# Performance work log

Measured on AMD Instinct MI355X. Metric: run time of the kernel, lower is better.

The kernel has to match this reference:

```python
import jax, jax.numpy as jnp
import numpy as np

T, B, P, D = 64, 32, 9, 512  # turns, batch, parties(=N_s), D_u=D_k=D_h


def setup_inputs() -> dict:
    key = jax.random.key(0)
    ks = jax.random.split(key, 12)
    f = lambda k, s: jax.random.normal(k, s, dtype=jnp.float32)
    sc = 0.02
    spk = jax.random.randint(ks[5], (T, B), 0, P)
    return {
        "U": f(ks[0], (T, B, D)), "SK": f(ks[1], (T, B, D)),
        "NU": f(ks[2], (T, B, D)), "LK": f(ks[3], (T, B, D)),
        "A": f(ks[4], (T, B, D)),
        "qmask": jax.nn.one_hot(spk, P, dtype=jnp.float32),  # one-hot party mask [T,B,P]
        # 4 Attention blocks (state11,state12,state21,state22): w_k, w_q, proj (D->D each)
        "Wk": f(ks[6], (4, D, D)) * sc, "bk": jnp.zeros((4, D), jnp.float32),
        "Wq": f(ks[7], (4, D, D)) * sc, "bq": jnp.zeros((4, D), jnp.float32),
        "Wp": f(ks[8], (4, D, D)) * sc, "bp": jnp.zeros((4, D), jnp.float32),
        # per-speaker GRUCell weights (dict of GRUCells -> stacked [P, ...], torch gate order r,z,n)
        "Wih": f(ks[9], (P, 3 * D, D)) * sc, "Whh": f(ks[10], (P, 3 * D, D)) * sc,
        "bih": jnp.zeros((P, 3 * D), jnp.float32), "bhh": jnp.zeros((P, 3 * D), jnp.float32),
    }


def reference(U, SK, NU, LK, A, qmask, Wk, bk, Wq, bq, Wp, bp, Wih, Whh, bih, bhh):
    Tn, Bn, Dn = U.shape
    Pn = qmask.shape[-1]
    bidx = jnp.arange(Bn)

    def attn(i, k2, q2):
        # Attention(D_k), n_head=1, score_function='dot_product', dropout=0 (eval)
        kx = k2 @ Wk[i].T + bk[i]                 # [B, D]
        qx = q2 @ Wq[i].T + bq[i]                 # [B, D]
        # k_len=q_len=1 -> score = <qx_b, kx_b>; original softmaxes over dim=0 (the batch axis!)
        score = jax.nn.softmax(jnp.sum(qx * kx, axis=-1), axis=0)  # [B]
        return (score[:, None] * kx) @ Wp[i].T + bp[i]  # [B, D]

    def gru(x, h, idx):
        # dynamically-routed per-speaker GRUCell: gather speaker weights, batched matvec
        gi = jnp.einsum('bd,bkd->bk', x, Wih[idx]) + bih[idx]  # [B, 3D]
        gh = jnp.einsum('bd,bkd->bk', h, Whh[idx]) + bhh[idx]
        ir, iz, inn = jnp.split(gi, 3, axis=-1)
        hr, hz, hn = jnp.split(gh, 3, axis=-1)
        r = jax.nn.sigmoid(ir + hr)
        z = jax.nn.sigmoid(iz + hz)
        n = jnp.tanh(inn + r * hn)
        return (1.0 - z) * n + z * h

    # qmask_n[t] = qmask[t+1] (next speaker), last repeats
    qmask_n = jnp.concatenate([qmask[1:], qmask[-1:]], axis=0)

    def step(s, xs):
        u, sk, nu, lk, qm, qmn = xs
        qi = jnp.argmax(qm, axis=1)   # speaker id per sample
        qni = jnp.argmax(qmn, axis=1)  # listener (next speaker) id
        s0s = s[bidx, qi]              # _select_parties
        s0l = s[bidx, qni]
        s_0 = attn(0, sk, u)
        s_s = attn(1, sk, s_0)
        s_1 = attn(2, lk, nu)
        s_l = attn(3, lk, s_1)
        spk = gru(s_s, s0s, qi)        # speaker state update
        lst = gru(s_l, s0l, qni)       # listener state update
        s_full = jnp.zeros_like(s).at[bidx, qi].set(spk)   # scatter_ dim=1
        l_full = jnp.zeros_like(s).at[bidx, qni].set(lst)
        s_new = (s * (1.0 - qm[..., None] - qmn[..., None])
                 + s_full * qm[..., None] + l_full * qmn[..., None])
        return s_new, s_new[bidx, qi]  # emit selected speaker state

    s0 = jnp.zeros((Bn, Pn, Dn), U.dtype)
    _, outs = jax.lax.scan(step, s0, (U, SK, NU, LK, qmask, qmask_n))
    # s_ starts as zeros(1, B, D_h) and concatenates per-step selections -> [T+1, B, D]
    return jnp.concatenate([jnp.zeros((1, Bn, Dn), U.dtype), outs], axis=0)
```

## Files before the change

### kernel.cpp

```cpp
#include <hip/hip_runtime.h>
#include <math.h>

#define Tn 64
#define Bn 32
#define Pn 9
#define Dn 512
#define TBn 2048
#define G3 1536
#define NCH 16

using short8 = __attribute__((ext_vector_type(8))) short;
using f32x4  = __attribute__((ext_vector_type(4))) float;
typedef unsigned long long ull;
typedef unsigned int uint;

__device__ __forceinline__ float fsigmoid(float x){ return 1.0f/(1.0f+__expf(-x)); }
__device__ __forceinline__ ushort f2bf(float x){
  unsigned u = __float_as_uint(x);
  return (ushort)((u + 0x7FFFu + ((u>>16)&1u)) >> 16);
}
__device__ __forceinline__ float bf2f(ushort h){
  return __uint_as_float(((unsigned)h)<<16);
}
__device__ __forceinline__ uint pk32(float x){
  ushort h = f2bf(x);
  ushort l = f2bf(x - bf2f(h));
  return ((uint)h << 16) | (uint)l;
}

__device__ __forceinline__ ull ld_agent8(const ull* p){
  return __hip_atomic_load(p, __ATOMIC_RELAXED, __HIP_MEMORY_SCOPE_AGENT);
}
__device__ __forceinline__ void st_agent8(ull* p, ull v){
  __hip_atomic_store(p, v, __ATOMIC_RELAXED, __HIP_MEMORY_SCOPE_AGENT);
}
__device__ __forceinline__ unsigned ld_agent4(const int* p){
  return (unsigned)__hip_atomic_load(p, __ATOMIC_RELAXED, __HIP_MEMORY_SCOPE_AGENT);
}
__device__ __forceinline__ void st_agent4(int* p, int v){
  __hip_atomic_store(p, v, __ATOMIC_RELAXED, __HIP_MEMORY_SCOPE_AGENT);
}
__device__ __forceinline__ float ulo(ull v){ return __uint_as_float((unsigned)v); }
__device__ __forceinline__ float uhi(ull v){ return __uint_as_float((unsigned)(v>>32)); }
__device__ __forceinline__ ull upack(float a, float b){
  return ((ull)__float_as_uint(b) << 32) | (ull)__float_as_uint(a);
}

__global__ void k_prep(const float* __restrict__ qmask, int* __restrict__ qi,
                       int* __restrict__ qni, float* __restrict__ h0A,
                       float* __restrict__ h0B, float* __restrict__ out,
                       int* __restrict__ counts, int* __restrict__ lists,
                       int* __restrict__ dcnt, int* __restrict__ dlist,
                       int* __restrict__ rowflag){
  int t = blockIdx.x; int tid = threadIdx.x;
  int gidx = blockIdx.x*256 + tid;
  if (gidx < 16) counts[gidx] = 0;
  if (gidx < Bn*Pn*NCH) st_agent4(&rowflag[gidx], 0);
  for (int i=gidx; i<9*4096; i+=64*256) lists[i] = -1;
  __shared__ int qis[32], qnis[32];
  __shared__ int cnt9[9];
  if (tid < 9) cnt9[tid] = 0;
  if (tid < Bn){
    int b = tid;
    const float* qm = qmask + ((size_t)t*Bn + b)*Pn;
    int best = 0; float bv = qm[0];
    #pragma unroll
    for (int p=1;p<Pn;p++){ float v=qm[p]; if (v>bv){bv=v;best=p;} }
    qi[t*Bn+b] = best; qis[b] = best;
    int tn = (t==Tn-1)? t : t+1;
    const float* qmn = qmask + ((size_t)tn*Bn + b)*Pn;
    best = 0; bv = qmn[0];
    #pragma unroll
    for (int p=1;p<Pn;p++){ float v=qmn[p]; if (v>bv){bv=v;best=p;} }
    qni[t*Bn+b] = best; qnis[b] = best;
  }
  __syncthreads();
  if (tid < Bn){
    int sp = qis[tid], lp = qnis[tid];
    if (sp == lp){
      int i = atomicAdd(&cnt9[sp], 1);
      dlist[(t*9+sp)*32 + i] = tid | 256 | 512;
    } else {
      int i = atomicAdd(&cnt9[sp], 1);
      dlist[(t*9+sp)*32 + i] = tid | 256;
      int j = atomicAdd(&cnt9[lp], 1);
      dlist[(t*9+lp)*32 + j] = tid | 512;
    }
  }
  __syncthreads();
  if (tid < 9) dcnt[t*9+tid] = cnt9[tid];
  for (int i=tid; i<2304; i+=256){ h0A[t*2304 + i] = 0.f; h0B[t*2304 + i] = 0.f; }
  for (int i=tid; i<256;  i+=256) out[t*256 + i] = 0.f;
}

__global__ void k_aux(const int* __restrict__ qi, const int* __restrict__ qni,
                      int* __restrict__ counts, int* __restrict__ lists,
                      const int* __restrict__ dcnt, int* __restrict__ dlist){
  int tid = threadIdx.x;
  if (blockIdx.x < 16){
    int id = blockIdx.x*256 + tid;
    int role = id >> 11, tb = id & (TBn-1);
    int p = role ? qni[tb] : qi[tb];
    int slot = atomicAdd(&counts[p], 1);
    lists[p*4096 + slot] = id;
  } else {
    for (int idx = tid; idx < Bn*Pn; idx += 256){
      int b = idx / Pn, pp = idx % Pn;
      int v = 0;
      for (int t=0;t<Tn;t++){
        if (qi[t*Bn+b]==pp || qni[t*Bn+b]==pp){
          int nn = dcnt[t*9+pp];
          int base = (t*9+pp)*32;
          for (int i=0;i<nn;i++){
            if ((dlist[base+i] & 31) == b){ dlist[base+i] |= (v<<16); break; }
          }
          v++;
        }
      }
    }
  }
}

struct PkD { const float* s; ushort* d; int n; };
__global__ __launch_bounds__(256) void k_packB(PkD p0, PkD p1, PkD p2, PkD p3,
                                               PkD p4, PkD p5, PkD p6, PkD p7){
  PkD D;
  switch (blockIdx.z){
    case 0: D=p0; break; case 1: D=p1; break; case 2: D=p2; break; case 3: D=p3; break;
    case 4: D=p4; break; case 5: D=p5; break; case 6: D=p6; break; default: D=p7; break;
  }
  int total = D.n * 128;
  for (int idx = blockIdx.x*256 + threadIdx.x; idx < total; idx += gridDim.x*256){
    int r = idx >> 7, c4 = idx & 127;
    float4 v = ((const float4*)D.s)[idx];
    ushort h0=f2bf(v.x), h1=f2bf(v.y), h2=f2bf(v.z), h3=f2bf(v.w);
    ushort l0=f2bf(v.x-bf2f(h0)), l1=f2bf(v.y-bf2f(h1)),
           l2=f2bf(v.z-bf2f(h2)), l3=f2bf(v.w-bf2f(h3));
    ushort* base = D.d + (size_t)r*1024;
    *(ushort4*)(base + c4*4)       = make_ushort4(h0,h1,h2,h3);
    *(ushort4*)(base + 512 + c4*4) = make_ushort4(l0,l1,l2,l3);
  }
}

struct MMd {
  const ushort* A; const ushort* B; float* C; const float* bias; ushort* Cpk;
  int asr, ahi, alo, bsr, bhi, blo, ldc, gx;
};
__global__ __launch_bounds__(256) void k_mmB(MMd d0, MMd d1, MMd d2, MMd d3){
  MMd d;
  switch (blockIdx.z){
    case 0: d=d0; break; case 1: d=d1; break; case 2: d=d2; break; default: d=d3; break;
  }
  if ((int)blockIdx.x >= d.gx) return;
  __shared__ ushort AshH[64*64];
  __shared__ ushort AshL[64*64];
  __shared__ ushort BshH[64*64];
  __shared__ ushort BshL[64*64];
  int bm = blockIdx.y*64, bn = blockIdx.x*64;
  int tid = threadIdx.x;
  int lane = tid & 63, w = tid >> 6;
  int wm = (w>>1)*32, wn = (w&1)*32;
  f32x4 acc[2][2] = {};
  int r0 = tid >> 3, g0 = tid & 7;
  int r1 = r0 + 32;
  const ushort* Ah = d.A + d.ahi;
  const ushort* Al = d.A + d.alo;
  const ushort* Bh = d.B + d.bhi;
  const ushort* Bl = d.B + d.blo;
  for (int k0=0; k0<512; k0+=64){
    short8 vah0 = *(const short8*)(Ah + (size_t)(bm+r0)*d.asr + k0 + g0*8);
    short8 vah1 = *(const short8*)(Ah + (size_t)(bm+r1)*d.asr + k0 + g0*8);
    short8 val0 = *(const short8*)(Al + (size_t)(bm+r0)*d.asr + k0 + g0*8);
    short8 val1 = *(const short8*)(Al + (size_t)(bm+r1)*d.asr + k0 + g0*8);
    short8 vbh0 = *(const short8*)(Bh + (size_t)(bn+r0)*d.bsr + k0 + g0*8);
    short8 vbh1 = *(const short8*)(Bh + (size_t)(bn+r1)*d.bsr + k0 + g0*8);
    short8 vbl0 = *(const short8*)(Bl + (size_t)(bn+r0)*d.bsr + k0 + g0*8);
    short8 vbl1 = *(const short8*)(Bl + (size_t)(bn+r1)*d.bsr + k0 + g0*8);
    __syncthreads();
    *(short8*)(AshH + r0*64 + ((g0 ^ (r0&7))*8)) = vah0;
    *(short8*)(AshH + r1*64 + ((g0 ^ (r1&7))*8)) = vah1;
    *(short8*)(AshL + r0*64 + ((g0 ^ (r0&7))*8)) = val0;
    *(short8*)(AshL + r1*64 + ((g0 ^ (r1&7))*8)) = val1;
    *(short8*)(BshH + r0*64 + ((g0 ^ (r0&7))*8)) = vbh0;
    *(short8*)(BshH + r1*64 + ((g0 ^ (r1&7))*8)) = vbh1;
    *(short8*)(BshL + r0*64 + ((g0 ^ (r0&7))*8)) = vbl0;
    *(short8*)(BshL + r1*64 + ((g0 ^ (r1&7))*8)) = vbl1;
    __syncthreads();
    #pragma unroll
    for (int kk=0; kk<2; ++kk){
      int gs = kk*4 + (lane>>4);
      short8 afh[2], afl[2], bfh[2], bfl[2];
      #pragma unroll
      for (int mi=0; mi<2; ++mi){
        int row = wm + mi*16 + (lane&15);
        afh[mi] = *(const short8*)(AshH + row*64 + ((gs ^ (row&7))*8));
        afl[mi] = *(const short8*)(AshL + row*64 + ((gs ^ (row&7))*8));
      }
      #pragma unroll
      for (int ni=0; ni<2; ++ni){
        int row = wn + ni*16 + (lane&15);
        bfh[ni] = *(const short8*)(BshH + row*64 + ((gs ^ (row&7))*8));
        bfl[ni] = *(const short8*)(BshL + row*64 + ((gs ^ (row&7))*8));
      }
      #pragma unroll
      for (int mi=0; mi<2; ++mi)
        #pragma unroll
        for (int ni=0; ni<2; ++ni){
          acc[mi][ni] = __builtin_amdgcn_mfma_f32_16x16x32_bf16(afh[mi], bfh[ni], acc[mi][ni], 0,0,0);
          acc[mi][ni] = __builtin_amdgcn_mfma_f32_16x16x32_bf16(afh[mi], bfl[ni], acc[mi][ni], 0,0,0);
          acc[mi][ni] = __builtin_amdgcn_mfma_f32_16x16x32_bf16(afl[mi], bfh[ni], acc[mi][ni], 0,0,0);
        }
    }
  }
  #pragma unroll
  for (int mi=0; mi<2; ++mi){
    #pragma unroll
    for (int ni=0; ni<2; ++ni){
      #pragma unroll
      for (int i=0;i<4;i++){
        int row = bm + wm + mi*16 + (lane>>4)*4 + i;
        int col = bn + wn + ni*16 + (lane&15);
        float v = acc[mi][ni][i];
        if (d.bias) v += d.bias[col];
        if (d.C) d.C[(size_t)row*d.ldc + col] = v;
        if (d.Cpk){
          ushort h = f2bf(v);
          d.Cpk[(size_t)row*2*d.ldc + col] = h;
          d.Cpk[(size_t)row*2*d.ldc + d.ldc + col] = f2bf(v - bf2f(h));
        }
      }
    }
  }
}

__global__ __launch_bounds__(256) void k_mm_g(
    const ushort* __restrict__ Spk0, const ushort* __restrict__ Spk1,
    const ushort* __restrict__ Wihpk, const float* __restrict__ bih,
    const int* __restrict__ counts, const int* __restrict__ lists,
    float* __restrict__ gis, float* __restrict__ gil)
{
  int p = blockIdx.z;
  int mt = blockIdx.y;
  if (mt*64 >= counts[p]) return;
  int bn = blockIdx.x*64;
  __shared__ ushort AshH[64*64];
  __shared__ ushort AshL[64*64];
  __shared__ ushort BshH[64*64];
  __shared__ ushort BshL[64*64];
  __shared__ int rid[64];
  int tid = threadIdx.x;
  int lane = tid & 63, w = tid >> 6;
  int wm = (w>>1)*32, wn = (w&1)*32;
  if (tid < 64) rid[tid] = lists[p*4096 + mt*64 + tid];
  __syncthreads();
  f32x4 acc[2][2] = {};
  int r0 = tid >> 3, g0 = tid & 7;
  int r1 = r0 + 32;
  int id0 = rid[r0], id1 = rid[r1];
  const ushort* As0 = (id0 >= 0) ? (((id0>>11)? Spk1:Spk0) + (size_t)(id0 & (TBn-1))*1024) : nullptr;
  const ushort* As1 = (id1 >= 0) ? (((id1>>11)? Spk1:Spk0) + (size_t)(id1 & (TBn-1))*1024) : nullptr;
  const ushort* Wb  = Wihpk + (size_t)(p*G3 + bn)*1024;
  short8 zz = {0,0,0,0,0,0,0,0};
  for (int k0=0; k0<512; k0+=64){
    short8 vah0 = As0 ? *(const short8*)(As0 + k0 + g0*8)       : zz;
    short8 val0 = As0 ? *(const short8*)(As0 + 512 + k0 + g0*8) : zz;
    short8 vah1 = As1 ? *(const short8*)(As1 + k0 + g0*8)       : zz;
    short8 val1 = As1 ? *(const short8*)(As1 + 512 + k0 + g0*8) : zz;
    short8 vbh0 = *(const short8*)(Wb + (size_t)r0*1024 + k0 + g0*8);
    short8 vbl0 = *(const short8*)(Wb + (size_t)r0*1024 + 512 + k0 + g0*8);
    short8 vbh1 = *(const short8*)(Wb + (size_t)r1*1024 + k0 + g0*8);
    short8 vbl1 = *(const short8*)(Wb + (size_t)r1*1024 + 512 + k0 + g0*8);
    __syncthreads();
    *(short8*)(AshH + r0*64 + ((g0 ^ (r0&7))*8)) = vah0;
    *(short8*)(AshH + r1*64 + ((g0 ^ (r1&7))*8)) = vah1;
    *(short8*)(AshL + r0*64 + ((g0 ^ (r0&7))*8)) = val0;
    *(short8*)(AshL + r1*64 + ((g0 ^ (r1&7))*8)) = val1;
    *(short8*)(BshH + r0*64 + ((g0 ^ (r0&7))*8)) = vbh0;
    *(short8*)(BshH + r1*64 + ((g0 ^ (r1&7))*8)) = vbh1;
    *(short8*)(BshL + r0*64 + ((g0 ^ (r0&7))*8)) = vbl0;
    *(short8*)(BshL + r1*64 + ((g0 ^ (r1&7))*8)) = vbl1;
    __syncthreads();
    #pragma unroll
    for (int kk=0; kk<2; ++kk){
      int gs = kk*4 + (lane>>4);
      short8 afh[2], afl[2], bfh[2], bfl[2];
      #pragma unroll
      for (int mi=0; mi<2; ++mi){
        int row = wm + mi*16 + (lane&15);
        afh[mi] = *(const short8*)(AshH + row*64 + ((gs ^ (row&7))*8));
        afl[mi] = *(const short8*)(AshL + row*64 + ((gs ^ (row&7))*8));
      }
      #pragma unroll
      for (int ni=0; ni<2; ++ni){
        int row = wn + ni*16 + (lane&15);
        bfh[ni] = *(const short8*)(BshH + row*64 + ((gs ^ (row&7))*8));
        bfl[ni] = *(const short8*)(BshL + row*64 + ((gs ^ (row&7))*8));
      }
      #pragma unroll
      for (int mi=0; mi<2; ++mi)
        #pragma unroll
        for (int ni=0; ni<2; ++ni){
          acc[mi][ni] = __builtin_amdgcn_mfma_f32_16x16x32_bf16(afh[mi], bfh[ni], acc[mi][ni], 0,0,0);
          acc[mi][ni] = __builtin_amdgcn_mfma_f32_16x16x32_bf16(afh[mi], bfl[ni], acc[mi][ni], 0,0,0);
          acc[mi][ni] = __builtin_amdgcn_mfma_f32_16x16x32_bf16(afl[mi], bfh[ni], acc[mi][ni], 0,0,0);
        }
    }
  }
  #pragma unroll
  for (int mi=0; mi<2; ++mi){
    #pragma unroll
    for (int ni=0; ni<2; ++ni){
      #pragma unroll
      for (int i=0;i<4;i++){
        int lrow = wm + mi*16 + (lane>>4)*4 + i;
        int id = rid[lrow];
        if (id < 0) continue;
        int col = bn + wn + ni*16 + (lane&15);
        float v = acc[mi][ni][i] + bih[p*G3 + col];
        float* dst = ((id>>11) ? gil : gis) + (size_t)(id & (TBn-1))*G3;
        dst[col] = v;
      }
    }
  }
}

__global__ __launch_bounds__(256) void k_scoreB(
      const float* __restrict__ qx0, const ushort* __restrict__ kh0,
      const ushort* __restrict__ kl0, const float* __restrict__ px0,
      const float* __restrict__ bp0, ushort* __restrict__ sp0,
      const float* __restrict__ qx1, const ushort* __restrict__ kh1,
      const ushort* __restrict__ kl1, const float* __restrict__ px1,
      const float* __restrict__ bp1, ushort* __restrict__ sp1, int ksr){
  const float* qx; const ushort* khi; const ushort* klo;
  const float* pkx; const float* bp; ushort* spk;
  if (blockIdx.y == 0){ qx=qx0; khi=kh0; klo=kl0; pkx=px0; bp=bp0; spk=sp0; }
  else                { qx=qx1; khi=kh1; klo=kl1; pkx=px1; bp=bp1; spk=sp1; }
  int t = blockIdx.x; int tid = threadIdx.x;
  __shared__ float part[256];
  __shared__ float dots[32];
  __shared__ float sc[32];
  int b = tid >> 3, j = tid & 7;
  const float* q = qx + ((size_t)t*Bn + b)*Dn;
  const ushort* kh = khi + ((size_t)t*Bn + b)*ksr;
  const ushort* kl = klo + ((size_t)t*Bn + b)*ksr;
  float s = 0.f;
  for (int d=j; d<Dn; d+=8) s = fmaf(q[d], bf2f(kh[d]) + bf2f(kl[d]), s);
  part[tid] = s;
  __syncthreads();
  if (tid < 32){
    float acc = 0.f;
    #pragma unroll
    for (int jj=0;jj<8;jj++) acc += part[tid*8+jj];
    dots[tid] = acc;
  }
  __syncthreads();
  if (tid < 32){
    float mx = dots[0];
    for (int o=1;o<32;o++) mx = fmaxf(mx, dots[o]);
    sc[tid] = __expf(dots[tid] - mx);
  }
  __syncthreads();
  float myscore = 0.f;
  if (tid < 32){
    float sum = 0.f;
    for (int o=0;o<32;o++) sum += sc[o];
    myscore = sc[tid] / sum;
  }
  __syncthreads();
  if (tid < 32) sc[tid] = myscore;
  __syncthreads();
  for (int idx=tid; idx<Bn*Dn; idx+=256){
    int bb = idx >> 9, d = idx & (Dn-1);
    float v = fmaf(sc[bb], pkx[((size_t)t*Bn+bb)*Dn + d], bp[d]);
    ushort h = f2bf(v);
    size_t o = ((size_t)t*Bn+bb)*1024 + d;
    spk[o] = h;
    spk[o + 512] = f2bf(v - bf2f(h));
  }
}

#define DC 32
#define NT 6
__global__ __launch_bounds__(512, 1) void k_rec(
    float* hA, float* hB,
    const int* __restrict__ dcnt, const int* __restrict__ dlist,
    const float* __restrict__ Whh, const float* __restrict__ bhh,
    const float* __restrict__ gis, const float* __restrict__ gil,
    float* __restrict__ out, int* rowflag){
  int p  = blockIdx.x;
  int ci = blockIdx.y;
  int d0 = ci * DC;
  int tid = threadIdx.x;
  int wave = tid >> 6, lane = tid & 63;

  __shared__ float4 hsh4[16][130];
  __shared__ uint   ab16[16][516];
  __shared__ float  ghs[16][97];
  __shared__ int    dls[32];

  short8 Bh[16], Bl[16];
  if (wave < NT){
    int wrow = wave*16 + (lane & 15);
    int grow = (wrow >> 5)*Dn + d0 + (wrow & 31);
    const float* wsrc = Whh + ((size_t)p*G3 + grow)*Dn + (lane>>4)*8;
    #pragma unroll
    for (int ks=0; ks<16; ++ks){
      float4 w0 = *(const float4*)(wsrc + ks*32);
      float4 w1 = *(const float4*)(wsrc + ks*32 + 4);
      float xs[8] = {w0.x,w0.y,w0.z,w0.w,w1.x,w1.y,w1.z,w1.w};
      #pragma unroll
      for (int j=0;j<8;j++){
        ushort hh = f2bf(xs[j]);
        Bh[ks][j] = (short)hh;
        Bl[ks][j] = (short)f2bf(xs[j] - bf2f(hh));
      }
    }
  }
  int dd0 = (tid & 15)*2, dfix = d0 + dd0;
  float bhr0 = bhh[p*G3 + dfix],        bhr1 = bhh[p*G3 + dfix + 1];
  float bhz0 = bhh[p*G3 + Dn + dfix],   bhz1 = bhh[p*G3 + Dn + dfix + 1];
  float bhn0 = bhh[p*G3 + 2*Dn + dfix], bhn1 = bhh[p*G3 + 2*Dn + dfix + 1];

  int entC = 0;
  if (tid < 32) entC = dlist[(0*9 + p)*32 + tid];

  for (int t=0; t<Tn; ++t){
    __syncthreads();
    if (tid < 32) dls[tid] = entC;
    __syncthreads();
    if (t+1 < Tn && tid < 32) entC = dlist[((t+1)*9 + p)*32 + tid];
    int n = dcnt[t*9+p];
    if (!n) continue;

    float pg[12];
    {
      int i = tid >> 4;
      if (i < n && i < 16){
        int ent = dls[i]; int b = ent & 31;
        if (ent & 256){
          const float* gS = gis + (size_t)(t*Bn + b)*G3;
          pg[0]=gS[dfix]; pg[1]=gS[dfix+1]; pg[2]=gS[Dn+dfix]; pg[3]=gS[Dn+dfix+1];
          pg[4]=gS[2*Dn+dfix]; pg[5]=gS[2*Dn+dfix+1];
        }
        if (ent & 512){
          const float* gL = gil + (size_t)(t*Bn + b)*G3;
          pg[6]=gL[dfix]; pg[7]=gL[dfix+1]; pg[8]=gL[Dn+dfix]; pg[9]=gL[Dn+dfix+1];
          pg[10]=gL[2*Dn+dfix]; pg[11]=gL[2*Dn+dfix+1];
        }
      }
    }

    {
      int i0 = wave*4 + (lane >> 4);
      if (i0 < n){
        int ent = dls[i0];
        unsigned need = (unsigned)(ent >> 16);
        if (need){
          int b = ent & 31;
          const int* cell = &rowflag[(b*Pn + p)*NCH + (lane & 15)];
          while (ld_agent4(cell) < need) __builtin_amdgcn_s_sleep(1);
        }
      }
    }
    __syncthreads();

    for (int g0=0; g0<n; g0+=16){
      int gn = n - g0; if (gn > 16) gn = 16;
      for (int idx=tid; idx<gn*128; idx+=512){
        int r = idx >> 7, q = idx & 127;
        int ent = dls[g0+r];
        int b = ent & 31;
        const float* hsrc = ((ent>>16) & 1) ? hB : hA;
        const ull* src = (const ull*)(hsrc + ((size_t)b*Pn + p)*Dn) + q*2;
        ull v0 = ld_agent8(src), v1 = ld_agent8(src+1);
        float4 f; f.x = ulo(v0); f.y = uhi(v0); f.z = ulo(v1); f.w = uhi(v1);
        hsh4[r][q ^ ((q>>3)&7)] = f;
        uint4 pk; pk.x = pk32(f.x); pk.y = pk32(f.y); pk.z = pk32(f.z); pk.w = pk32(f.w);
        *(uint4*)&ab16[r][q*4] = pk;
      }
      __syncthreads();

      if (wave < NT){
        f32x4 acc = {0.f,0.f,0.f,0.f};
        int arow = lane & 15;
        int kq   = (lane >> 4)*8;
        #pragma unroll
        for (int ks=0; ks<16; ++ks){
          uint4 u0 = *(const uint4*)&ab16[arow][ks*32 + kq];
          uint4 u1 = *(const uint4*)&ab16[arow][ks*32 + kq + 4];
          uint uu[8] = {u0.x,u0.y,u0.z,u0.w,u1.x,u1.y,u1.z,u1.w};
          short8 Ah, Al;
          #pragma unroll
          for (int j=0;j<8;j++){
            Ah[j] = (short)(uu[j] >> 16);
            Al[j] = (short)(uu[j] & 0xffffu);
          }
          acc = __builtin_amdgcn_mfma_f32_16x16x32_bf16(Ah, Bh[ks], acc, 0,0,0);
          acc = __builtin_amdgcn_mfma_f32_16x16x32_bf16(Ah, Bl[ks], acc, 0,0,0);
          acc = __builtin_amdgcn_mfma_f32_16x16x32_bf16(Al, Bh[ks], acc, 0,0,0);
        }
        #pragma unroll
        for (int i=0;i<4;i++)
          ghs[(lane>>4)*4 + i][wave*16 + (lane & 15)] = acc[i];
      }
      __syncthreads();

      if (tid < gn*16){
        int i = tid >> 4;
        int ent = dls[g0+i];
        int b = ent & 31;
        bool S = (ent & 256) != 0, L = (ent & 512) != 0;
        int v = ent >> 16;
        float* hdst = (v & 1) ? hA : hB;
        int qq = dfix >> 2;
        float4 u = hsh4[i][qq ^ ((qq>>3)&7)];
        float hv0 = (dfix & 2) ? u.z : u.x;
        float hv1 = (dfix & 2) ? u.w : u.y;
        float ghr0 = ghs[i][dd0]    + bhr0, ghr1 = ghs[i][dd0+1]    + bhr1;
        float ghz0 = ghs[i][32+dd0] + bhz0, ghz1 = ghs[i][32+dd0+1] + bhz1;
        float ghn0 = ghs[i][64+dd0] + bhn0, ghn1 = ghs[i][64+dd0+1] + bhn1;
        float v0 = hv0, v1 = hv1;
        if (S){
          float i0,i1,i2,i3,i4,i5;
          if (g0 == 0){ i0=pg[0]; i1=pg[1]; i2=pg[2]; i3=pg[3]; i4=pg[4]; i5=pg[5]; }
          else {
            const float* gS = gis + (size_t)(t*Bn + b)*G3;
            i0=gS[dfix]; i1=gS[dfix+1]; i2=gS[Dn+dfix]; i3=gS[Dn+dfix+1];
            i4=gS[2*Dn+dfix]; i5=gS[2*Dn+dfix+1];
          }
          float rg0 = fsigmoid(i0 + ghr0), rg1 = fsigmoid(i1 + ghr1);
          float zg0 = fsigmoid(i2 + ghz0), zg1 = fsigmoid(i3 + ghz1);
          float ng0 = tanhf(fmaf(rg0, ghn0, i4));
          float ng1 = tanhf(fmaf(rg1, ghn1, i5));
          v0 = fmaf(zg0, hv0 - ng0, ng0);
          v1 = fmaf(zg1, hv1 - ng1, ng1);
        }
        if (L){
          float i0,i1,i2,i3,i4,i5;
          if (g0 == 0){ i0=pg[6]; i1=pg[7]; i2=pg[8]; i3=pg[9]; i4=pg[10]; i5=pg[11]; }
          else {
            const float* gL = gil + (size_t)(t*Bn + b)*G3;
            i0=gL[dfix]; i1=gL[dfix+1]; i2=gL[Dn+dfix]; i3=gL[Dn+dfix+1];
            i4=gL[2*Dn+dfix]; i5=gL[2*Dn+dfix+1];
          }
          float rg0 = fsigmoid(i0 + ghr0), rg1 = fsigmoid(i1 + ghr1);
          float zg0 = fsigmoid(i2 + ghz0), zg1 = fsigmoid(i3 + ghz1);
          float ng0 = tanhf(fmaf(rg0, ghn0, i4));
          float ng1 = tanhf(fmaf(rg1, ghn1, i5));
          float hl0 = fmaf(zg0, hv0 - ng0, ng0);
          float hl1 = fmaf(zg1, hv1 - ng1, ng1);
          if (S){ v0 += hl0 - hv0; v1 += hl1 - hv1; }
          else  { v0 = hl0; v1 = hl1; }
        }
        st_agent8((ull*)(hdst + ((size_t)b*Pn + p)*Dn + dfix), upack(v0, v1));
        if (S) *(ull*)(out + ((size_t)(t+1)*Bn + b)*Dn + dfix) = upack(v0, v1);
      }
      __syncthreads();
    }

    if (tid < n){
      int ent = dls[tid];
      st_agent4(&rowflag[((ent & 31)*Pn + p)*NCH + ci], (ent >> 16) + 1);
    }
  }
}

extern "C" void kernel_launch(void* const* d_in, const int* in_sizes, int n_in,
                              void* d_out, int out_size, void* d_ws, size_t ws_size,
                              hipStream_t stream){
  const float* U    = (const float*)d_in[0];
  const float* SK   = (const float*)d_in[1];
  const float* NU   = (const float*)d_in[2];
  const float* LK   = (const float*)d_in[3];
  const float* qmask= (const float*)d_in[5];
  const float* bk   = (const float*)d_in[7];
  const float* bq   = (const float*)d_in[9];
  const float* bp   = (const float*)d_in[11];
  const float* Wk   = (const float*)d_in[6];
  const float* Wq   = (const float*)d_in[8];
  const float* Wp   = (const float*)d_in[10];
  const float* Wih  = (const float*)d_in[12];
  const float* Whh  = (const float*)d_in[13];
  const float* bih  = (const float*)d_in[14];
  const float* bhh  = (const float*)d_in[15];
  float* out = (float*)d_out;

  char* w = (char*)d_ws;
  size_t off = 0;
  auto alloc = [&](size_t bytes)->void*{ void* p = w + off; off += (bytes + 255) & ~(size_t)255; return p; };
  ushort* SKpk = (ushort*)alloc(2048UL*1024*2);
  ushort* LKpk = (ushort*)alloc(2048UL*1024*2);
  ushort* Upk  = (ushort*)alloc(2048UL*1024*2);
  ushort* NUpk = (ushort*)alloc(2048UL*1024*2);
  ushort* Wkpk = (ushort*)alloc(2048UL*1024*2);
  ushort* Wqpk = (ushort*)alloc(2048UL*1024*2);
  ushort* Wppk = (ushort*)alloc(2048UL*1024*2);
  ushort* Wihpk= (ushort*)alloc(13824UL*1024*2);
  ushort* kxApk= (ushort*)alloc(2048UL*2048*2);
  ushort* kxBpk= (ushort*)alloc(2048UL*2048*2);
  float* qxA   = (float*)alloc(2048UL*512*4);
  float* qxB   = (float*)alloc(2048UL*512*4);
  ushort* s0pk = (ushort*)alloc(2048UL*1024*2);
  ushort* s1pk = (ushort*)alloc(2048UL*1024*2);
  float* gis   = (float*)alloc(2048UL*1536*4);
  float* gil   = (float*)alloc(2048UL*1536*4);
  float* hA    = (float*)alloc(32UL*9*512*4);
  float* hB    = (float*)alloc(32UL*9*512*4);
  int* qi      = (int*)alloc(2048*4);
  int* qni     = (int*)alloc(2048*4);
  int* counts  = (int*)alloc(16*4);
  int* lists   = (int*)alloc(9*4096*4);
  int* dcnt    = (int*)alloc(64*9*4);
  int* dlist   = (int*)alloc(64*9*32*4);
  int* rowflag = (int*)alloc(32*9*NCH*4);
  float* pkx0 = (float*)(void*)SKpk;
  float* pkx1 = (float*)(void*)LKpk;
  float* pkx2 = (float*)(void*)Upk;
  float* pkx3 = (float*)(void*)NUpk;
  (void)ws_size; (void)in_sizes; (void)n_in; (void)out_size;

  dim3 blk(256);

  k_prep<<<64, blk, 0, stream>>>(qmask, qi, qni, hA, hB, out, counts, lists, dcnt, dlist, rowflag);
  k_aux <<<17, blk, 0, stream>>>(qi, qni, counts, lists, dcnt, dlist);

  {
    PkD p0{SK, SKpk, 2048}, p1{LK, LKpk, 2048}, p2{U, Upk, 2048}, p3{NU, NUpk, 2048};
    PkD p4{Wk, Wkpk, 2048}, p5{Wq, Wqpk, 2048}, p6{Wp, Wppk, 2048}, p7{Wih, Wihpk, 13824};
    k_packB<<<dim3(256,1,8), blk, 0, stream>>>(p0,p1,p2,p3,p4,p5,p6,p7);
  }

  {
    MMd d0{SKpk, Wkpk,                       nullptr, bk,      kxApk, 1024,0,512, 1024,0,512, 1024, 16};
    MMd d1{LKpk, Wkpk+(size_t)1024*1024,     nullptr, bk+1024, kxBpk, 1024,0,512, 1024,0,512, 1024, 16};
    MMd d2{Upk,  Wqpk,                       qxA,     bq,      nullptr,1024,0,512, 1024,0,512, 512,  8};
    MMd d3{NUpk, Wqpk+(size_t)1024*1024,     qxB,     bq+1024, nullptr,1024,0,512, 1024,0,512, 512,  8};
    k_mmB<<<dim3(16,32,4), blk, 0, stream>>>(d0,d1,d2,d3);
  }
  {
    MMd d0{kxApk, Wppk,                      pkx0, nullptr, nullptr, 2048,0,  1024, 1024,0,512, 512, 8};
    MMd d1{kxApk, Wppk+(size_t)512*1024,     pkx1, nullptr, nullptr, 2048,512,1536, 1024,0,512, 512, 8};
    MMd d2{kxBpk, Wppk+(size_t)1024*1024,    pkx2, nullptr, nullptr, 2048,0,  1024, 1024,0,512, 512, 8};
    MMd d3{kxBpk, Wppk+(size_t)1536*1024,    pkx3, nullptr, nullptr, 2048,512,1536, 1024,0,512, 512, 8};
    k_mmB<<<dim3(8,32,4), blk, 0, stream>>>(d0,d1,d2,d3);
  }

  k_scoreB<<<dim3(64,2), blk, 0, stream>>>(qxA, kxApk+0, kxApk+1024, pkx0, bp,      s0pk,
                                           qxB, kxBpk+0, kxBpk+1024, pkx2, bp+1024, s1pk, 2048);

  {
    MMd d0{s0pk, Wqpk+(size_t)512*1024,  qxA, bq+512,  nullptr, 1024,0,512, 1024,0,512, 512, 8};
    MMd d1{s1pk, Wqpk+(size_t)1536*1024, qxB, bq+1536, nullptr, 1024,0,512, 1024,0,512, 512, 8};
    k_mmB<<<dim3(8,32,2), blk, 0, stream>>>(d0,d1,d0,d0);
  }

  k_scoreB<<<dim3(64,2), blk, 0, stream>>>(qxA, kxApk+512, kxApk+1536, pkx1, bp+512,  s0pk,
                                           qxB, kxBpk+512, kxBpk+1536, pkx3, bp+1536, s1pk, 2048);

  k_mm_g<<<dim3(24,64,9), blk, 0, stream>>>(s0pk, s1pk, Wihpk, bih, counts, lists, gis, gil);

  k_rec<<<dim3(9,NCH), dim3(512), 0, stream>>>(hA, hB, dcnt, dlist, Whh, bhh, gis, gil, out, rowflag);
}
```

Baseline: 708.2 us.

## Refactor attention chain algebraically to remove score-dependent GEMM serialization

The second attention's query depends linearly on the first's softmax score, so the code precomputes Wq·Wp as a combined weight plus a bias vector. Both scores then come from dot products in one score kernel. The GRU input projection is applied to the unscaled Wp·kx and the per-row score is applied inside the recurrence, with precomputed constant terms C1 and C3. This removes one GEMM and one score kernel from the serial chain and lets the Wih GEMM run before the scores are known. In exchange it adds extra setup work, a transposed Wp pack and the Wq·Wp GEMM, plus a few FMAs and shared-memory loads in the recurrent kernel.

```diff
diff --git a/kernel.cpp b/kernel.cpp
--- a/kernel.cpp
+++ b/kernel.cpp
@@ -8,6 +8,7 @@
 #define TBn 2048
 #define G3 1536
 #define NCH 16
+#define DD2 262144
 
 using short8 = __attribute__((ext_vector_type(8))) short;
 using f32x4  = __attribute__((ext_vector_type(4))) float;
@@ -44,6 +45,11 @@
 __device__ __forceinline__ float uhi(ull v){ return __uint_as_float((unsigned)(v>>32)); }
 __device__ __forceinline__ ull upack(float a, float b){
   return ((ull)__float_as_uint(b) << 32) | (ull)__float_as_uint(a);
+}
+__device__ __forceinline__ float wave_red(float a){
+  a += __shfl_xor(a, 1);  a += __shfl_xor(a, 2);  a += __shfl_xor(a, 4);
+  a += __shfl_xor(a, 8);  a += __shfl_xor(a, 16); a += __shfl_xor(a, 32);
+  return a;
 }
 
 __global__ void k_prep(const float* __restrict__ qmask, int* __restrict__ qi,
@@ -93,17 +99,23 @@
   for (int i=tid; i<256;  i+=256) out[t*256 + i] = 0.f;
 }
 
-__global__ void k_aux(const int* __restrict__ qi, const int* __restrict__ qni,
-                      int* __restrict__ counts, int* __restrict__ lists,
-                      const int* __restrict__ dcnt, int* __restrict__ dlist){
-  int tid = threadIdx.x;
-  if (blockIdx.x < 16){
-    int id = blockIdx.x*256 + tid;
+__global__ __launch_bounds__(256) void k_aux(
+    const int* __restrict__ qi, const int* __restrict__ qni,
+    int* __restrict__ counts, int* __restrict__ lists,
+    const int* __restrict__ dcnt, int* __restrict__ dlist,
+    const float* __restrict__ Wq, const float* __restrict__ Wih,
+    const float* __restrict__ Wp, const float* __restrict__ bp,
+    const float* __restrict__ bq, const float* __restrict__ bih,
+    ushort* __restrict__ WpTpk, float* __restrict__ cvec,
+    float* __restrict__ C1, float* __restrict__ C3){
+  int bx = blockIdx.x, tid = threadIdx.x;
+  if (bx < 16){
+    int id = bx*256 + tid;
     int role = id >> 11, tb = id & (TBn-1);
     int p = role ? qni[tb] : qi[tb];
     int slot = atomicAdd(&counts[p], 1);
     lists[p*4096 + slot] = id;
-  } else {
+  } else if (bx == 16){
     for (int idx = tid; idx < Bn*Pn; idx += 256){
       int b = idx / Pn, pp = idx % Pn;
       int v = 0;
@@ -116,6 +128,49 @@
           }
           v++;
         }
+      }
+    }
+  } else if (bx < 33){
+    int g = (bx-17)*256 + tid;
+    int r = g >> 3, cb = (g & 7)*64;
+    #pragma unroll
+    for (int mi=0; mi<2; mi++){
+      const float* src = Wp + (size_t)mi*2*DD2;
+      ushort* dst = WpTpk + (size_t)(mi*512 + r)*1024;
+      for (int c=cb; c<cb+64; c++){
+        float v = src[(size_t)c*512 + r];
+        ushort h = f2bf(v);
+        dst[c] = h; dst[512+c] = f2bf(v - bf2f(h));
+      }
+    }
+  } else {
+    int wv = (bx-33)*4 + (tid>>6), lane = tid & 63;
+    if (wv < 16){
+      for (int i=0;i<64;i++){
+        int r = wv*64 + i;
+        int m = r >> 9, j = r & 511;
+        const float* wrow = Wq + (size_t)(m?3:1)*DD2 + (size_t)j*512;
+        const float* bpv  = bp + (m? 1024 : 0);
+        float acc = 0.f;
+        #pragma unroll
+        for (int e=0;e<8;e++) acc = fmaf(wrow[lane*8+e], bpv[lane*8+e], acc);
+        acc = wave_red(acc);
+        if (lane==0) cvec[r] = acc + bq[(m?1536:512) + j];
+      }
+    } else if (wv < 232){
+      int base = (wv-16)*64;
+      for (int i=0;i<64;i++){
+        int r = base + i;
+        const float* wrow = Wih + (size_t)r*512;
+        float a1=0.f, a3=0.f;
+        #pragma unroll
+        for (int e=0;e<8;e++){
+          float wv8 = wrow[lane*8+e];
+          a1 = fmaf(wv8, bp[512 + lane*8+e], a1);
+          a3 = fmaf(wv8, bp[1536 + lane*8+e], a3);
+        }
+        a1 = wave_red(a1); a3 = wave_red(a3);
+        if (lane==0){ C1[r] = a1 + bih[r]; C3[r] = a3 + bih[r]; }
       }
     }
   }
@@ -235,7 +290,7 @@
 
 __global__ __launch_bounds__(256) void k_mm_g(
     const ushort* __restrict__ Spk0, const ushort* __restrict__ Spk1,
-    const ushort* __restrict__ Wihpk, const float* __restrict__ bih,
+    const ushort* __restrict__ Wihpk,
     const int* __restrict__ counts, const int* __restrict__ lists,
     float* __restrict__ gis, float* __restrict__ gil)
 {
@@ -312,70 +367,70 @@
     for (int ni=0; ni<2; ++ni){
       #pragma unroll
       for (int i=0;i<4;i++){
-        int lrow = wm + mi*16 + (lane>>4)*4 + i;
-        int id = rid[lrow];
+        int lrow2 = wm + mi*16 + (lane>>4)*4 + i;
+        int id = rid[lrow2];
         if (id < 0) continue;
         int col = bn + wn + ni*16 + (lane&15);
-        float v = acc[mi][ni][i] + bih[p*G3 + col];
         float* dst = ((id>>11) ? gil : gis) + (size_t)(id & (TBn-1))*G3;
-        dst[col] = v;
-      }
-    }
-  }
-}
-
-__global__ __launch_bounds__(256) void k_scoreB(
-      const float* __restrict__ qx0, const ushort* __restrict__ kh0,
-      const ushort* __restrict__ kl0, const float* __restrict__ px0,
-      const float* __restrict__ bp0, ushort* __restrict__ sp0,
-      const float* __restrict__ qx1, const ushort* __restrict__ kh1,
-      const ushort* __restrict__ kl1, const float* __restrict__ px1,
-      const float* __restrict__ bp1, ushort* __restrict__ sp1, int ksr){
-  const float* qx; const ushort* khi; const ushort* klo;
-  const float* pkx; const float* bp; ushort* spk;
-  if (blockIdx.y == 0){ qx=qx0; khi=kh0; klo=kl0; pkx=px0; bp=bp0; spk=sp0; }
-  else                { qx=qx1; khi=kh1; klo=kl1; pkx=px1; bp=bp1; spk=sp1; }
-  int t = blockIdx.x; int tid = threadIdx.x;
-  __shared__ float part[256];
-  __shared__ float dots[32];
-  __shared__ float sc[32];
-  int b = tid >> 3, j = tid & 7;
-  const float* q = qx + ((size_t)t*Bn + b)*Dn;
-  const ushort* kh = khi + ((size_t)t*Bn + b)*ksr;
-  const ushort* kl = klo + ((size_t)t*Bn + b)*ksr;
-  float s = 0.f;
-  for (int d=j; d<Dn; d+=8) s = fmaf(q[d], bf2f(kh[d]) + bf2f(kl[d]), s);
-  part[tid] = s;
+        dst[col] = acc[mi][ni][i];
+      }
+    }
+  }
+}
+
+__global__ __launch_bounds__(256) void k_scoreT(
+    const float* __restrict__ qx0, const ushort* __restrict__ kxA,
+    const float* __restrict__ qq1,
+    const float* __restrict__ qx2, const ushort* __restrict__ kxB,
+    const float* __restrict__ qq3,
+    const float* __restrict__ cvec, float* __restrict__ scS,
+    float* __restrict__ scL){
+  int t = blockIdx.x, side = blockIdx.y, tid = threadIdx.x;
+  const float* qx; const ushort* kx; const float* qq; const float* cv; float* sco;
+  if (side==0){ qx=qx0; kx=kxA; qq=qq1; cv=cvec;     sco=scS; }
+  else        { qx=qx2; kx=kxB; qq=qq3; cv=cvec+512; sco=scL; }
+  __shared__ float p0[256], pA[256], pB[256];
+  __shared__ float d0s[32], dAs[32], dBs[32], es[32], e1[32];
+  int b = tid>>3, j = tid&7;
+  const float* q   = qx + (size_t)(t*Bn+b)*Dn;
+  const float* qqr = qq + (size_t)(t*Bn+b)*Dn;
+  const ushort* kr = kx + (size_t)(t*Bn+b)*2048;
+  float s0=0.f, sA=0.f, sB=0.f;
+  for (int d=j; d<Dn; d+=8){
+    float k0v = bf2f(kr[d])     + bf2f(kr[1024+d]);
+    float k1v = bf2f(kr[512+d]) + bf2f(kr[1536+d]);
+    s0 = fmaf(q[d],   k0v, s0);
+    sA = fmaf(qqr[d], k1v, sA);
+    sB = fmaf(cv[d],  k1v, sB);
+  }
+  p0[tid]=s0; pA[tid]=sA; pB[tid]=sB;
   __syncthreads();
   if (tid < 32){
-    float acc = 0.f;
-    #pragma unroll
-    for (int jj=0;jj<8;jj++) acc += part[tid*8+jj];
-    dots[tid] = acc;
+    float a0=0,aA=0,aB=0;
+    #pragma unroll
+    for (int jj=0;jj<8;jj++){ a0+=p0[tid*8+jj]; aA+=pA[tid*8+jj]; aB+=pB[tid*8+jj]; }
+    d0s[tid]=a0; dAs[tid]=aA; dBs[tid]=aB;
   }
   __syncthreads();
   if (tid < 32){
-    float mx = dots[0];
-    for (int o=1;o<32;o++) mx = fmaxf(mx, dots[o]);
-    sc[tid] = __expf(dots[tid] - mx);
+    float mx=d0s[0]; for(int o=1;o<32;o++) mx=fmaxf(mx,d0s[o]);
+    es[tid]=__expf(d0s[tid]-mx);
   }
   __syncthreads();
-  float myscore = 0.f;
   if (tid < 32){
-    float sum = 0.f;
-    for (int o=0;o<32;o++) sum += sc[o];
-    myscore = sc[tid] / sum;
+    float sum=0; for(int o=0;o<32;o++) sum+=es[o];
+    float sc0 = es[tid]/sum;
+    e1[tid] = fmaf(sc0, dAs[tid], dBs[tid]);
   }
   __syncthreads();
-  if (tid < 32) sc[tid] = myscore;
+  if (tid < 32){
+    float mx=e1[0]; for(int o=1;o<32;o++) mx=fmaxf(mx,e1[o]);
+    es[tid]=__expf(e1[tid]-mx);
+  }
   __syncthreads();
-  for (int idx=tid; idx<Bn*Dn; idx+=256){
-    int bb = idx >> 9, d = idx & (Dn-1);
-    float v = fmaf(sc[bb], pkx[((size_t)t*Bn+bb)*Dn + d], bp[d]);
-    ushort h = f2bf(v);
-    size_t o = ((size_t)t*Bn+bb)*1024 + d;
-    spk[o] = h;
-    spk[o + 512] = f2bf(v - bf2f(h));
+  if (tid < 32){
+    float sum=0; for(int o=0;o<32;o++) sum+=es[o];
+    sco[t*Bn+tid] = es[tid]/sum;
   }
 }
 
@@ -386,6 +441,8 @@
     const int* __restrict__ dcnt, const int* __restrict__ dlist,
     const float* __restrict__ Whh, const float* __restrict__ bhh,
     const float* __restrict__ gis, const float* __restrict__ gil,
+    const float* __restrict__ scS, const float* __restrict__ scL,
+    const float* __restrict__ C1, const float* __restrict__ C3,
     float* __restrict__ out, int* rowflag){
   int p  = blockIdx.x;
   int ci = blockIdx.y;
@@ -397,6 +454,9 @@
   __shared__ uint   ab16[16][516];
   __shared__ float  ghs[16][97];
   __shared__ int    dls[32];
+  __shared__ float  scSsh[TBn], scLsh[TBn];
+
+  for (int i=tid; i<TBn; i+=512){ scSsh[i]=scS[i]; scLsh[i]=scL[i]; }
 
   short8 Bh[16], Bl[16];
   if (wave < NT){
@@ -420,6 +480,16 @@
   float bhr0 = bhh[p*G3 + dfix],        bhr1 = bhh[p*G3 + dfix + 1];
   float bhz0 = bhh[p*G3 + Dn + dfix],   bhz1 = bhh[p*G3 + Dn + dfix + 1];
   float bhn0 = bhh[p*G3 + 2*Dn + dfix], bhn1 = bhh[p*G3 + 2*Dn + dfix + 1];
+  float c1v[6], c3v[6];
+  {
+    const float* C1p = C1 + p*G3; const float* C3p = C3 + p*G3;
+    c1v[0]=C1p[dfix];        c1v[1]=C1p[dfix+1];
+    c1v[2]=C1p[Dn+dfix];     c1v[3]=C1p[Dn+dfix+1];
+    c1v[4]=C1p[2*Dn+dfix];   c1v[5]=C1p[2*Dn+dfix+1];
+    c3v[0]=C3p[dfix];        c3v[1]=C3p[dfix+1];
+    c3v[2]=C3p[Dn+dfix];     c3v[3]=C3p[Dn+dfix+1];
+    c3v[4]=C3p[2*Dn+dfix];   c3v[5]=C3p[2*Dn+dfix+1];
+  }
 
   int entC = 0;
   if (tid < 32) entC = dlist[(0*9 + p)*32 + tid];
@@ -521,13 +591,17 @@
         float ghn0 = ghs[i][64+dd0] + bhn0, ghn1 = ghs[i][64+dd0+1] + bhn1;
         float v0 = hv0, v1 = hv1;
         if (S){
-          float i0,i1,i2,i3,i4,i5;
-          if (g0 == 0){ i0=pg[0]; i1=pg[1]; i2=pg[2]; i3=pg[3]; i4=pg[4]; i5=pg[5]; }
+          float g0v,g1v,g2v,g3v,g4v,g5v;
+          if (g0 == 0){ g0v=pg[0]; g1v=pg[1]; g2v=pg[2]; g3v=pg[3]; g4v=pg[4]; g5v=pg[5]; }
           else {
             const float* gS = gis + (size_t)(t*Bn + b)*G3;
-            i0=gS[dfix]; i1=gS[dfix+1]; i2=gS[Dn+dfix]; i3=gS[Dn+dfix+1];
-            i4=gS[2*Dn+dfix]; i5=gS[2*Dn+dfix+1];
+            g0v=gS[dfix]; g1v=gS[dfix+1]; g2v=gS[Dn+dfix]; g3v=gS[Dn+dfix+1];
+            g4v=gS[2*Dn+dfix]; g5v=gS[2*Dn+dfix+1];
           }
+          float sc = scSsh[t*Bn + b];
+          float i0 = fmaf(sc, g0v, c1v[0]), i1 = fmaf(sc, g1v, c1v[1]);
+          float i2 = fmaf(sc, g2v, c1v[2]), i3 = fmaf(sc, g3v, c1v[3]);
+          float i4 = fmaf(sc, g4v, c1v[4]), i5 = fmaf(sc, g5v, c1v[5]);
           float rg0 = fsigmoid(i0 + ghr0), rg1 = fsigmoid(i1 + ghr1);
           float zg0 = fsigmoid(i2 + ghz0), zg1 = fsigmoid(i3 + ghz1);
           float ng0 = tanhf(fmaf(rg0, ghn0, i4));
@@ -536,13 +610,17 @@
           v1 = fmaf(zg1, hv1 - ng1, ng1);
         }
         if (L){
-          float i0,i1,i2,i3,i4,i5;
-          if (g0 == 0){ i0=pg[6]; i1=pg[7]; i2=pg[8]; i3=pg[9]; i4=pg[10]; i5=pg[11]; }
+          float g0v,g1v,g2v,g3v,g4v,g5v;
+          if (g0 == 0){ g0v=pg[6]; g1v=pg[7]; g2v=pg[8]; g3v=pg[9]; g4v=pg[10]; g5v=pg[11]; }
           else {
             const float* gL = gil + (size_t)(t*Bn + b)*G3;
-            i0=gL[dfix]; i1=gL[dfix+1]; i2=gL[Dn+dfix]; i3=gL[Dn+dfix+1];
-            i4=gL[2*Dn+dfix]; i5=gL[2*Dn+dfix+1];
+            g0v=gL[dfix]; g1v=gL[dfix+1]; g2v=gL[Dn+dfix]; g3v=gL[Dn+dfix+1];
+            g4v=gL[2*Dn+dfix]; g5v=gL[2*Dn+dfix+1];
           }
+          float sc = scLsh[t*Bn + b];
+          float i0 = fmaf(sc, g0v, c3v[0]), i1 = fmaf(sc, g1v, c3v[1]);
+          float i2 = fmaf(sc, g2v, c3v[2]), i3 = fmaf(sc, g3v, c3v[3]);
+          float i4 = fmaf(sc, g4v, c3v[4]), i5 = fmaf(sc, g5v, c3v[5]);
           float rg0 = fsigmoid(i0 + ghr0), rg1 = fsigmoid(i1 + ghr1);
           float zg0 = fsigmoid(i2 + ghz0), zg1 = fsigmoid(i3 + ghz1);
           float ng0 = tanhf(fmaf(rg0, ghn0, i4));
@@ -588,41 +666,47 @@
   char* w = (char*)d_ws;
   size_t off = 0;
   auto alloc = [&](size_t bytes)->void*{ void* p = w + off; off += (bytes + 255) & ~(size_t)255; return p; };
-  ushort* SKpk = (ushort*)alloc(2048UL*1024*2);
-  ushort* LKpk = (ushort*)alloc(2048UL*1024*2);
-  ushort* Upk  = (ushort*)alloc(2048UL*1024*2);
-  ushort* NUpk = (ushort*)alloc(2048UL*1024*2);
-  ushort* Wkpk = (ushort*)alloc(2048UL*1024*2);
-  ushort* Wqpk = (ushort*)alloc(2048UL*1024*2);
-  ushort* Wppk = (ushort*)alloc(2048UL*1024*2);
-  ushort* Wihpk= (ushort*)alloc(13824UL*1024*2);
-  ushort* kxApk= (ushort*)alloc(2048UL*2048*2);
-  ushort* kxBpk= (ushort*)alloc(2048UL*2048*2);
-  float* qxA   = (float*)alloc(2048UL*512*4);
-  float* qxB   = (float*)alloc(2048UL*512*4);
-  ushort* s0pk = (ushort*)alloc(2048UL*1024*2);
-  ushort* s1pk = (ushort*)alloc(2048UL*1024*2);
-  float* gis   = (float*)alloc(2048UL*1536*4);
-  float* gil   = (float*)alloc(2048UL*1536*4);
-  float* hA    = (float*)alloc(32UL*9*512*4);
-  float* hB    = (float*)alloc(32UL*9*512*4);
-  int* qi      = (int*)alloc(2048*4);
-  int* qni     = (int*)alloc(2048*4);
-  int* counts  = (int*)alloc(16*4);
-  int* lists   = (int*)alloc(9*4096*4);
-  int* dcnt    = (int*)alloc(64*9*4);
-  int* dlist   = (int*)alloc(64*9*32*4);
-  int* rowflag = (int*)alloc(32*9*NCH*4);
-  float* pkx0 = (float*)(void*)SKpk;
-  float* pkx1 = (float*)(void*)LKpk;
-  float* pkx2 = (float*)(void*)Upk;
-  float* pkx3 = (float*)(void*)NUpk;
+  ushort* SKpk  = (ushort*)alloc(2048UL*1024*2);
+  ushort* LKpk  = (ushort*)alloc(2048UL*1024*2);
+  ushort* Upk   = (ushort*)alloc(2048UL*1024*2);
+  ushort* NUpk  = (ushort*)alloc(2048UL*1024*2);
+  ushort* Wkpk  = (ushort*)alloc(2048UL*1024*2);
+  ushort* Wqpk  = (ushort*)alloc(2048UL*1024*2);
+  ushort* Wppk  = (ushort*)alloc(2048UL*1024*2);
+  ushort* Wihpk = (ushort*)alloc(13824UL*1024*2);
+  ushort* WpTpk = (ushort*)alloc(1024UL*1024*2);
+  ushort* WWpk  = (ushort*)alloc(1024UL*1024*2);
+  ushort* kxApk = (ushort*)alloc(2048UL*2048*2);
+  ushort* kxBpk = (ushort*)alloc(2048UL*2048*2);
+  ushort* pkx1pk= (ushort*)alloc(2048UL*1024*2);
+  ushort* pkx3pk= (ushort*)alloc(2048UL*1024*2);
+  float* qxA    = (float*)alloc(2048UL*512*4);
+  float* qxB    = (float*)alloc(2048UL*512*4);
+  float* qq1    = (float*)alloc(2048UL*512*4);
+  float* qq3    = (float*)alloc(2048UL*512*4);
+  float* gis    = (float*)alloc(2048UL*1536*4);
+  float* gil    = (float*)alloc(2048UL*1536*4);
+  float* hA     = (float*)alloc(32UL*9*512*4);
+  float* hB     = (float*)alloc(32UL*9*512*4);
+  float* cvec   = (float*)alloc(1024*4);
+  float* C1     = (float*)alloc(9UL*1536*4);
+  float* C3     = (float*)alloc(9UL*1536*4);
+  float* scS    = (float*)alloc(2048*4);
+  float* scL    = (float*)alloc(2048*4);
+  int* qi       = (int*)alloc(2048*4);
+  int* qni      = (int*)alloc(2048*4);
+  int* counts   = (int*)alloc(16*4);
+  int* lists    = (int*)alloc(9*4096*4);
+  int* dcnt     = (int*)alloc(64*9*4);
+  int* dlist    = (int*)alloc(64*9*32*4);
+  int* rowflag  = (int*)alloc(32*9*NCH*4);
   (void)ws_size; (void)in_sizes; (void)n_in; (void)out_size;
 
   dim3 blk(256);
 
   k_prep<<<64, blk, 0, stream>>>(qmask, qi, qni, hA, hB, out, counts, lists, dcnt, dlist, rowflag);
-  k_aux <<<17, blk, 0, stream>>>(qi, qni, counts, lists, dcnt, dlist);
+  k_aux <<<91, blk, 0, stream>>>(qi, qni, counts, lists, dcnt, dlist,
+                                 Wq, Wih, Wp, bp, bq, bih, WpTpk, cvec, C1, C3);
 
   {
     PkD p0{SK, SKpk, 2048}, p1{LK, LKpk, 2048}, p2{U, Upk, 2048}, p3{NU, NUpk, 2048};
@@ -631,33 +715,33 @@
   }
 
   {
-    MMd d0{SKpk, Wkpk,                       nullptr, bk,      kxApk, 1024,0,512, 1024,0,512, 1024, 16};
-    MMd d1{LKpk, Wkpk+(size_t)1024*1024,     nullptr, bk+1024, kxBpk, 1024,0,512, 1024,0,512, 1024, 16};
-    MMd d2{Upk,  Wqpk,                       qxA,     bq,      nullptr,1024,0,512, 1024,0,512, 512,  8};
-    MMd d3{NUpk, Wqpk+(size_t)1024*1024,     qxB,     bq+1024, nullptr,1024,0,512, 1024,0,512, 512,  8};
+    MMd d0{Wqpk+(size_t)512*1024,  WpTpk,                 nullptr, nullptr, WWpk,
+           1024,0,512, 1024,0,512, 512, 8};
+    MMd d1{Wqpk+(size_t)1536*1024, WpTpk+(size_t)512*1024, nullptr, nullptr, WWpk+(size_t)512*1024,
+           1024,0,512, 1024,0,512, 512, 8};
+    k_mmB<<<dim3(8,8,2), blk, 0, stream>>>(d0,d1,d0,d0);
+  }
+
+  {
+    MMd d0{SKpk, Wkpk,                   nullptr, bk,      kxApk, 1024,0,512, 1024,0,512, 1024, 16};
+    MMd d1{LKpk, Wkpk+(size_t)1024*1024, nullptr, bk+1024, kxBpk, 1024,0,512, 1024,0,512, 1024, 16};
+    MMd d2{Upk,  Wqpk,                   qxA,     bq,      nullptr,1024,0,512, 1024,0,512, 512,  8};
+    MMd d3{NUpk, Wqpk+(size_t)1024*1024, qxB,     bq+1024, nullptr,1024,0,512, 1024,0,512, 512,  8};
     k_mmB<<<dim3(16,32,4), blk, 0, stream>>>(d0,d1,d2,d3);
   }
+
   {
-    MMd d0{kxApk, Wppk,                      pkx0, nullptr, nullptr, 2048,0,  1024, 1024,0,512, 512, 8};
-    MMd d1{kxApk, Wppk+(size_t)512*1024,     pkx1, nullptr, nullptr, 2048,512,1536, 1024,0,512, 512, 8};
-    MMd d2{kxBpk, Wppk+(size_t)1024*1024,    pkx2, nullptr, nullptr, 2048,0,  1024, 1024,0,512, 512, 8};
-    MMd d3{kxBpk, Wppk+(size_t)1536*1024,    pkx3, nullptr, nullptr, 2048,512,1536, 1024,0,512, 512, 8};
+    MMd d0{kxApk, Wppk+(size_t)512*1024,  nullptr, nullptr, pkx1pk, 2048,512,1536, 1024,0,512, 512, 8};
+    MMd d1{kxBpk, Wppk+(size_t)1536*1024, nullptr, nullptr, pkx3pk, 2048,512,1536, 1024,0,512, 512, 8};
+    MMd d2{kxApk, WWpk,                   qq1,     nullptr, nullptr,2048,0,  1024, 1024,0,512, 512, 8};
+    MMd d3{kxBpk, WWpk+(size_t)512*1024,  qq3,     nullptr, nullptr,2048,0,  1024, 1024,0,512, 512, 8};
     k_mmB<<<dim3(8,32,4), blk, 0, stream>>>(d0,d1,d2,d3);
   }
 
-  k_scoreB<<<dim3(64,2), blk, 0, stream>>>(qxA, kxApk+0, kxApk+1024, pkx0, bp,      s0pk,
-                                           qxB, kxBpk+0, kxBpk+1024, pkx2, bp+1024, s1pk, 2048);
-
-  {
-    MMd d0{s0pk, Wqpk+(size_t)512*1024,  qxA, bq+512,  nullptr, 1024,0,512, 1024,0,512, 512, 8};
-    MMd d1{s1pk, Wqpk+(size_t)1536*1024, qxB, bq+1536, nullptr, 1024,0,512, 1024,0,512, 512, 8};
-    k_mmB<<<dim3(8,32,2), blk, 0, stream>>>(d0,d1,d0,d0);
-  }
-
-  k_scoreB<<<dim3(64,2), blk, 0, stream>>>(qxA, kxApk+512, kxApk+1536, pkx1, bp+512,  s0pk,
-                                           qxB, kxBpk+512, kxBpk+1536, pkx3, bp+1536, s1pk, 2048);
-
-  k_mm_g<<<dim3(24,64,9), blk, 0, stream>>>(s0pk, s1pk, Wihpk, bih, counts, lists, gis, gil);
-
-  k_rec<<<dim3(9,NCH), dim3(512), 0, stream>>>(hA, hB, dcnt, dlist, Whh, bhh, gis, gil, out, rowflag);
-}
+  k_mm_g<<<dim3(24,64,9), blk, 0, stream>>>(pkx1pk, pkx3pk, Wihpk, counts, lists, gis, gil);
+
+  k_scoreT<<<dim3(64,2), blk, 0, stream>>>(qxA, kxApk, qq1, qxB, kxBpk, qq3, cvec, scS, scL);
+
+  k_rec<<<dim3(9,NCH), dim3(512), 0, stream>>>(hA, hB, dcnt, dlist, Whh, bhh,
+                                               gis, gil, scS, scL, C1, C3, out, rowflag);
+}
```

Result: faster. 653.9 us (-7.7%).
